# Performance work log

Measured on AMD Instinct MI355X. Metric: run time of the kernel, lower is better.

Reference implementation:

```python
import jax, jax.numpy as jnp
import numpy as np

# PyTorch LSTM gate order: i, f, g, o. Dropout layers are identity in eval mode.

def _lstm_step(w_ih, w_hh, b):
    def step(carry, xt):
        h, c = carry
        g = xt @ w_ih.T + h @ w_hh.T + b
        i, f, gg, o = jnp.split(g, 4, axis=-1)
        c = jax.nn.sigmoid(f) * c + jax.nn.sigmoid(i) * jnp.tanh(gg)
        h = jax.nn.sigmoid(o) * jnp.tanh(c)
        return (h, c), h
    return step


def bilstm(x, wf_ih, wf_hh, bf_ih, bf_hh, wb_ih, wb_hh, bb_ih, bb_hh):
    # x: [B, T, D] -> out: [B, T, 2H]
    B = x.shape[0]
    H = wf_hh.shape[1]
    xt = jnp.swapaxes(x, 0, 1)  # [T, B, D]
    init = (jnp.zeros((B, H), x.dtype), jnp.zeros((B, H), x.dtype))
    _, hf = jax.lax.scan(_lstm_step(wf_ih, wf_hh, bf_ih + bf_hh), init, xt)
    _, hb = jax.lax.scan(_lstm_step(wb_ih, wb_hh, bb_ih + bb_hh), init, xt[::-1])
    hb = hb[::-1]
    return jnp.swapaxes(jnp.concatenate([hf, hb], axis=-1), 0, 1)


def setup_inputs() -> dict:
    key = jax.random.key(0)
    ks = iter(jax.random.split(key, 64))
    d = {"x": jax.random.normal(next(ks), (1024, 1024, 8), jnp.float32)}
    layer_dims = [(16, 20), (40, 20), (40, 10), (20, 10)]
    for li, (din, H) in enumerate(layer_dims, start=1):
        for dr in ("f", "b"):
            d[f"w{li}{dr}_ih"] = 0.1 * jax.random.normal(next(ks), (4 * H, din), jnp.float32)
            d[f"w{li}{dr}_hh"] = 0.1 * jax.random.normal(next(ks), (4 * H, H), jnp.float32)
            d[f"b{li}{dr}_ih"] = 0.1 * jax.random.normal(next(ks), (4 * H,), jnp.float32)
            d[f"b{li}{dr}_hh"] = 0.1 * jax.random.normal(next(ks), (4 * H,), jnp.float32)
    d["fc_w"] = 0.1 * jax.random.normal(next(ks), (1, 20), jnp.float32)
    d["fc_b"] = 0.1 * jax.random.normal(next(ks), (1,), jnp.float32)
    return d


def reference(x,
              w1f_ih, w1f_hh, b1f_ih, b1f_hh, w1b_ih, w1b_hh, b1b_ih, b1b_hh,
              w2f_ih, w2f_hh, b2f_ih, b2f_hh, w2b_ih, w2b_hh, b2b_ih, b2b_hh,
              w3f_ih, w3f_hh, b3f_ih, b3f_hh, w3b_ih, w3b_hh, b3b_ih, b3b_hh,
              w4f_ih, w4f_hh, b4f_ih, b4f_hh, w4b_ih, w4b_hh, b4b_ih, b4b_hh,
              fc_w, fc_b):
    # lag-1 concat: [B,T,8] -> [B,T,16]
    x_lag = jnp.concatenate([jnp.zeros_like(x[:, :1, :]), x[:, :-1, :]], axis=1)
    h = jnp.concatenate([x, x_lag], axis=2)
    h = bilstm(h, w1f_ih, w1f_hh, b1f_ih, b1f_hh, w1b_ih, w1b_hh, b1b_ih, b1b_hh)
    h = bilstm(h, w2f_ih, w2f_hh, b2f_ih, b2f_hh, w2b_ih, w2b_hh, b2b_ih, b2b_hh)
    h = bilstm(h, w3f_ih, w3f_hh, b3f_ih, b3f_hh, w3b_ih, w3b_hh, b3b_ih, b3b_hh)
    h = bilstm(h, w4f_ih, w4f_hh, b4f_ih, b4f_hh, w4b_ih, w4b_hh, b4b_ih, b4b_hh)
    h = h[:, -1, :]  # [B, 20]
    return jax.nn.sigmoid(h @ fc_w.T + fc_b)
```

## Files before the change

### kernel.cpp

```cpp
#include <hip/hip_runtime.h>
#include <hip/hip_fp16.h>
#include <stdint.h>

#define B_TOTAL 1024
#define T_TOTAL 1024
#define LOG2E 1.44269504088896f

typedef _Float16 f16x2 __attribute__((ext_vector_type(2)));

__device__ __forceinline__ float dot2w(uint32_t xw, uint32_t ww, float acc) {
#if __has_builtin(__builtin_amdgcn_fdot2)
    return __builtin_amdgcn_fdot2(__builtin_bit_cast(f16x2, xw),
                                  __builtin_bit_cast(f16x2, ww), acc, false);
#else
    f16x2 xv = __builtin_bit_cast(f16x2, xw);
    f16x2 wv = __builtin_bit_cast(f16x2, ww);
    return acc + (float)xv.x * (float)wv.x + (float)xv.y * (float)wv.y;
#endif
}

__device__ __forceinline__ uint32_t packf2(float a, float b) {
    f16x2 t;
    t.x = (_Float16)a;
    t.y = (_Float16)b;
    return __builtin_bit_cast(uint32_t, t);
}

__device__ __forceinline__ float sigm_(float z) {
    float e = __builtin_amdgcn_exp2f(-LOG2E * z);
    return __builtin_amdgcn_rcpf(1.0f + e);
}
__device__ __forceinline__ float tanh_(float z) {
    float e = __builtin_amdgcn_exp2f((2.0f * LOG2E) * z);
    float r = __builtin_amdgcn_rcpf(1.0f + e);
    return __builtin_fmaf(-2.0f, r, 1.0f);
}

__device__ __forceinline__ void wavebar() {
#if __has_builtin(__builtin_amdgcn_wave_barrier)
    __builtin_amdgcn_wave_barrier();
#endif
}

template <int DIN, int H, int NDIR, bool L1X>
__global__ void __launch_bounds__(256) proj_kernel(
    const float* __restrict__ x,
    const __half* __restrict__ inbuf,
    const float* __restrict__ w0,
    const float* __restrict__ w1,
    __half* __restrict__ g0,
    __half* __restrict__ g1,
    int t0, int seglen)
{
    constexpr int NDW = DIN / 2;
    constexpr int O4H = 4 * H;
    constexpr int ODW = O4H / 2;
    constexpr int RPB = 16;
    constexpr int TPR = 16;
    constexpr int OPT = (O4H + TPR - 1) / TPR;
    constexpr int TILES = 8;

    __shared__ uint32_t wt[NDW][O4H];
    __shared__ uint32_t xin[RPB * NDW];
    __shared__ uint32_t osm[RPB][ODW];

    const int tid  = threadIdx.x;
    const int dirz = (NDIR == 2) ? (int)blockIdx.y : 0;
    const float* w = dirz ? w1 : w0;
    __half* gout   = dirz ? g1 : g0;
    (void)seglen;

    for (int idx = tid; idx < NDW * O4H; idx += 256) {
        const int d  = idx / O4H;
        const int o  = idx - d * O4H;
        const int jj = o >> 2;
        const int qq = o & 3;
        wt[d][o] = packf2(w[(qq * H + jj) * DIN + 2 * d],
                          w[(qq * H + jj) * DIN + 2 * d + 1]);
    }

    const int rr = tid >> 4;
    const int li = tid & 15;

    for (int tile = 0; tile < TILES; ++tile) {
        const int r0 = ((int)blockIdx.x * TILES + tile) * RPB;
        __syncthreads();

        for (int idx = tid; idx < RPB * NDW; idx += 256) {
            const int r  = r0 + idx / NDW;
            const int d  = idx % NDW;
            const int i  = r >> 10;
            const int bb = r & (B_TOTAL - 1);
            const int t  = dirz ? (T_TOTAL - 1 - t0 - i) : (t0 + i);
            uint32_t v;
            if constexpr (L1X) {
                float2 u = {0.f, 0.f};
                if (d < 4)
                    u = ((const float2*)(x + ((size_t)bb * T_TOTAL + t) * 8))[d];
                else if (t > 0)
                    u = ((const float2*)(x + ((size_t)bb * T_TOTAL + (t - 1)) * 8))[d - 4];
                v = packf2(u.x, u.y);
            } else {
                v = ((const uint32_t*)inbuf)[((size_t)t * B_TOTAL + bb) * NDW + d];
            }
            xin[idx] = v;
        }
        __syncthreads();

        float acc[OPT];
#pragma unroll
        for (int oi = 0; oi < OPT; ++oi) acc[oi] = 0.f;
#pragma unroll
        for (int d = 0; d < NDW; ++d) {
            const uint32_t xv = xin[rr * NDW + d];
#pragma unroll
            for (int oi = 0; oi < OPT; ++oi) {
                const int o = li + oi * TPR;
                if (O4H % TPR == 0 || o < O4H)
                    acc[oi] = dot2w(xv, wt[d][o], acc[oi]);
            }
        }
        {
            __half* oh = (__half*)&osm[rr][0];
#pragma unroll
            for (int oi = 0; oi < OPT; ++oi) {
                const int o = li + oi * TPR;
                if (O4H % TPR == 0 || o < O4H) oh[o] = __float2half(acc[oi]);
            }
        }
        __syncthreads();

        {
            uint32_t* dst = (uint32_t*)gout;
            for (int idx = tid; idx < RPB * ODW; idx += 256) {
                const int r  = idx / ODW;
                const int od = idx - r * ODW;
                dst[(size_t)(r0 + r) * ODW + od] = osm[r][od];
            }
        }
    }
}

template <int H, bool STORE_ALL>
__global__ void __launch_bounds__(64)
__attribute__((amdgpu_waves_per_eu(1, 1))) lstm_scan2(
    const __half* __restrict__ gxf, const __half* __restrict__ gxb,
    const float* __restrict__ whhf, const float* __restrict__ bihf,
    const float* __restrict__ bhhf,
    const float* __restrict__ whhb, const float* __restrict__ bihb,
    const float* __restrict__ bhhb,
    __half* __restrict__ outbuf,
    float* __restrict__ lasth,
    float* __restrict__ sth, float* __restrict__ stc,
    int t0, int seglen)
{
    constexpr int GPW   = 64 / H;
    constexpr int NH    = H / 2;
    constexpr int HS_DW = (H == 20) ? 12 : 8;
    constexpr int PF    = 8;

    const int dir  = blockIdx.y;
    const int lane = threadIdx.x;
    const int g    = lane / H;
    const int j    = lane - g * H;
    const int b    = blockIdx.x * GPW + g;
    const bool valid = (g < GPW) && (b < B_TOTAL);
    const int bs   = valid ? b : (B_TOTAL - 1);

    const __half* gx  = dir ? gxb : gxf;
    const float* w_hh = dir ? whhb : whhf;
    const float* b_i  = dir ? bihb : bihf;
    const float* b_h  = dir ? bhhb : bhhf;

    __shared__ uint32_t hsm[GPW + 1][HS_DW];

    uint32_t whh2[4][NH];
    float bias[4];
#pragma unroll
    for (int q = 0; q < 4; ++q) {
        const int r = q * H + j;
#pragma unroll
        for (int k = 0; k < NH; ++k)
            whh2[q][k] = packf2(w_hh[r * H + 2 * k], w_hh[r * H + 2 * k + 1]);
        bias[q] = b_i[r] + b_h[r];
    }
#pragma unroll
    for (int q = 0; q < 4; ++q) {
#pragma unroll
        for (int k = 0; k < NH; ++k) asm volatile("" : "+v"(whh2[q][k]));
        asm volatile("" : "+v"(bias[q]));
    }

    float c_st, h0;
    if (t0 == 0) {
        c_st = 0.f;
        h0   = 0.f;
    } else {
        h0   = sth[((size_t)dir * B_TOTAL + bs) * H + j];
        c_st = stc[((size_t)dir * B_TOTAL + bs) * H + j];
    }
    ((__half*)&hsm[g][0])[j] = __float2half(h0);
    wavebar();

    uint32_t hd[NH];
    auto readhd = [&]() {
        const uint32_t* hp = &hsm[g][0];
        if constexpr (NH == 10) {
            uint4 v0 = *(const uint4*)hp;
            uint4 v1 = *(const uint4*)(hp + 4);
            uint2 v2 = *(const uint2*)(hp + 8);
            hd[0] = v0.x; hd[1] = v0.y; hd[2] = v0.z; hd[3] = v0.w;
            hd[4] = v1.x; hd[5] = v1.y; hd[6] = v1.z; hd[7] = v1.w;
            hd[8] = v2.x; hd[9] = v2.y;
        } else {
            uint4 v0 = *(const uint4*)hp;
            hd[0] = v0.x; hd[1] = v0.y; hd[2] = v0.z; hd[3] = v0.w;
            hd[4] = hp[4];
        }
    };
    readhd();

    const char*  gb   = (const char*)gx + ((size_t)bs * (4 * H) + (size_t)j * 4) * 2;
    const size_t ISTR = (size_t)B_TOTAL * (4 * H) * 2;

    uint2 pf[PF];
#pragma unroll
    for (int i2 = 0; i2 < PF; ++i2) {
        const int ip = (i2 < seglen) ? i2 : (seglen - 1);
        pf[i2] = *(const uint2*)(gb + (size_t)ip * ISTR);
    }

    __half* op = nullptr;
    ptrdiff_t opstep = 0;
    if constexpr (STORE_ALL) {
        const int tstart = dir ? (T_TOTAL - 1 - t0) : t0;
        op = outbuf + (size_t)tstart * (B_TOTAL * 2 * H) + (size_t)bs * (2 * H) + dir * H + j;
        opstep = (dir ? -1 : 1) * (ptrdiff_t)(B_TOTAL * 2 * H);
    }

    float hlast = h0;

#define STEP(I)                                                               \
    {                                                                         \
        const uint2 gv = pf[I];                                               \
        int ip = sb + (I) + PF;                                               \
        ip = (ip < seglen) ? ip : (seglen - 1);                               \
        pf[I] = *(const uint2*)(gb + (size_t)ip * ISTR);                      \
        const f16x2 p01 = __builtin_bit_cast(f16x2, gv.x);                    \
        const f16x2 p23 = __builtin_bit_cast(f16x2, gv.y);                    \
        float a0 = (float)p01.x + bias[0];                                    \
        float a1 = (float)p01.y + bias[1];                                    \
        float a2 = (float)p23.x + bias[2];                                    \
        float a3 = (float)p23.y + bias[3];                                    \
        _Pragma("unroll")                                                     \
        for (int k = 0; k < NH; ++k) {                                        \
            a0 = dot2w(hd[k], whh2[0][k], a0);                                \
            a1 = dot2w(hd[k], whh2[1][k], a1);                                \
            a2 = dot2w(hd[k], whh2[2][k], a2);                                \
            a3 = dot2w(hd[k], whh2[3][k], a3);                                \
        }                                                                     \
        const float iv = sigm_(a0);                                           \
        const float fv = sigm_(a1);                                           \
        const float gv2 = tanh_(a2);                                          \
        const float ov = sigm_(a3);                                           \
        c_st = __builtin_fmaf(fv, c_st, iv * gv2);                            \
        const float h = ov * tanh_(c_st);                                     \
        ((__half*)&hsm[g][0])[j] = __float2half(h);                           \
        wavebar();                                                            \
        readhd();                                                             \
        hlast = h;                                                            \
        if constexpr (STORE_ALL) {                                            \
            if (valid) *op = __float2half(h);                                 \
            op += opstep;                                                     \
        }                                                                     \
    }

    for (int sb = 0; sb < seglen; sb += PF) {
        STEP(0) STEP(1) STEP(2) STEP(3) STEP(4) STEP(5) STEP(6) STEP(7)
    }
#undef STEP

    if (valid) {
        sth[((size_t)dir * B_TOTAL + b) * H + j] = hlast;
        stc[((size_t)dir * B_TOTAL + b) * H + j] = c_st;
        if constexpr (!STORE_ALL) lasth[b * H + j] = hlast;
    }
}

__global__ void final_kernel(const __half* __restrict__ l3out,
                             const float* __restrict__ hf4,
                             const float* __restrict__ w_ih,
                             const float* __restrict__ b_ih,
                             const float* __restrict__ b_hh,
                             const float* __restrict__ fc_w,
                             const float* __restrict__ fc_b,
                             float* __restrict__ out)
{
    const int b = blockIdx.x * blockDim.x + threadIdx.x;
    if (b >= B_TOTAL) return;

    float in4[20];
    const __half* p = l3out + (size_t)(T_TOTAL - 1) * (B_TOTAL * 20) + (size_t)b * 20;
#pragma unroll
    for (int i = 0; i < 20; ++i) in4[i] = __half2float(p[i]);

    float z = fc_b[0];
#pragma unroll
    for (int k = 0; k < 10; ++k) z += fc_w[k] * hf4[b * 10 + k];

#pragma unroll
    for (int k = 0; k < 10; ++k) {
        float gi = b_ih[k]      + b_hh[k];
        float gg = b_ih[20 + k] + b_hh[20 + k];
        float go = b_ih[30 + k] + b_hh[30 + k];
#pragma unroll
        for (int i = 0; i < 20; ++i) {
            const float xi = in4[i];
            gi += w_ih[k * 20 + i]        * xi;
            gg += w_ih[(20 + k) * 20 + i] * xi;
            go += w_ih[(30 + k) * 20 + i] * xi;
        }
        const float cc = sigm_(gi) * tanh_(gg);
        const float hb = sigm_(go) * tanh_(cc);
        z += fc_w[10 + k] * hb;
    }
    out[b] = sigm_(z);
}

extern "C" void kernel_launch(void* const* d_in, const int* in_sizes, int n_in,
                              void* d_out, int out_size, void* d_ws, size_t ws_size,
                              hipStream_t stream) {
    const float* x = (const float*)d_in[0];
    auto W = [&](int li, int dr, int k) -> const float* {
        return (const float*)d_in[1 + (li - 1) * 8 + dr * 4 + k];
    };
    const float* fc_w = (const float*)d_in[33];
    const float* fc_b = (const float*)d_in[34];
    float* out = (float*)d_out;

    const size_t HA_B = (size_t)T_TOTAL * B_TOTAL * 40 * 2;
    const size_t HB_B = (size_t)T_TOTAL * B_TOTAL * 20 * 2;
    const size_t ST_B = 2ull * B_TOTAL * 20 * 4;
    const size_t F4_B = (size_t)B_TOTAL * 10 * 4;

    char* p = (char*)d_ws;
    __half* hA = (__half*)p;  p += HA_B;
    __half* hB = (__half*)p;  p += HB_B;
    float* sth = (float*)p;   p += ST_B;
    float* stc = (float*)p;   p += ST_B;
    float* hf4 = (float*)p;   p += F4_B;
    __half* gx = (__half*)p;

    const size_t base = HA_B + HB_B + 2 * ST_B + F4_B;
    int SEG = 64;
    if      (ws_size >= base + 1024ull * 327680) SEG = 1024;
    else if (ws_size >= base +  512ull * 327680) SEG = 512;
    else if (ws_size >= base +  256ull * 327680) SEG = 256;
    else if (ws_size >= base +  128ull * 327680) SEG = 128;
    const int nseg = T_TOTAL / SEG;

    auto g1of = [&](int H) { return gx + (size_t)SEG * 1024 * 4 * H; };

    for (int s = 0; s < nseg; ++s) {
        proj_kernel<16, 20, 2, true><<<dim3(SEG * 8, 2), 256, 0, stream>>>(
            x, nullptr, W(1,0,0), W(1,1,0), gx, g1of(20), s * SEG, SEG);
        lstm_scan2<20, true><<<dim3(342, 2), 64, 0, stream>>>(
            gx, g1of(20), W(1,0,1), W(1,0,2), W(1,0,3),
                          W(1,1,1), W(1,1,2), W(1,1,3),
            hA, nullptr, sth, stc, s * SEG, SEG);
    }
    for (int s = 0; s < nseg; ++s) {
        proj_kernel<40, 20, 2, false><<<dim3(SEG * 8, 2), 256, 0, stream>>>(
            nullptr, hA, W(2,0,0), W(2,1,0), gx, g1of(20), s * SEG, SEG);
        lstm_scan2<20, true><<<dim3(342, 2), 64, 0, stream>>>(
            gx, g1of(20), W(2,0,1), W(2,0,2), W(2,0,3),
                          W(2,1,1), W(2,1,2), W(2,1,3),
            hA, nullptr, sth, stc, s * SEG, SEG);
    }
    for (int s = 0; s < nseg; ++s) {
        proj_kernel<40, 10, 2, false><<<dim3(SEG * 8, 2), 256, 0, stream>>>(
            nullptr, hA, W(3,0,0), W(3,1,0), gx, g1of(10), s * SEG, SEG);
        lstm_scan2<10, true><<<dim3(171, 2), 64, 0, stream>>>(
            gx, g1of(10), W(3,0,1), W(3,0,2), W(3,0,3),
                          W(3,1,1), W(3,1,2), W(3,1,3),
            hB, nullptr, sth, stc, s * SEG, SEG);
    }
    for (int s = 0; s < nseg; ++s) {
        proj_kernel<20, 10, 1, false><<<dim3(SEG * 8, 1), 256, 0, stream>>>(
            nullptr, hB, W(4,0,0), W(4,0,0), gx, gx, s * SEG, SEG);
        lstm_scan2<10, false><<<dim3(171, 1), 64, 0, stream>>>(
            gx, gx, W(4,0,1), W(4,0,2), W(4,0,3),
                    W(4,0,1), W(4,0,2), W(4,0,3),
            nullptr, hf4, sth, stc, s * SEG, SEG);
    }

    final_kernel<<<dim3(4), 256, 0, stream>>>(
        hB, hf4, W(4,1,0), W(4,1,2), W(4,1,3), fc_w, fc_b, out);
}
```

Before: 1.801 ms.

## Interleave two independent batch groups per wave in LSTM scan, register-cache projection weights

Result: slower. 2.463 ms (+36.8%).

```diff
diff --git a/kernel.cpp b/kernel.cpp
--- a/kernel.cpp
+++ b/kernel.cpp
@@ -52,16 +52,17 @@
     __half* __restrict__ g1,
     int t0, int seglen)
 {
-    constexpr int NDW = DIN / 2;
-    constexpr int O4H = 4 * H;
-    constexpr int ODW = O4H / 2;
-    constexpr int RPB = 16;
-    constexpr int TPR = 16;
-    constexpr int OPT = (O4H + TPR - 1) / TPR;
+    constexpr int NDW  = DIN / 2;
+    constexpr int XPAD = (NDW + 3) & ~3;
+    constexpr int O4H  = 4 * H;
+    constexpr int ODW  = O4H / 2;
+    constexpr int RPB  = 16;
+    constexpr int TPR  = 16;
+    constexpr int OPT  = (O4H + TPR - 1) / TPR;
     constexpr int TILES = 8;
 
     __shared__ uint32_t wt[NDW][O4H];
-    __shared__ uint32_t xin[RPB * NDW];
+    __shared__ uint32_t xin[RPB * XPAD];
     __shared__ uint32_t osm[RPB][ODW];
 
     const int tid  = threadIdx.x;
@@ -78,17 +79,28 @@
         wt[d][o] = packf2(w[(qq * H + jj) * DIN + 2 * d],
                           w[(qq * H + jj) * DIN + 2 * d + 1]);
     }
+    __syncthreads();
 
     const int rr = tid >> 4;
     const int li = tid & 15;
+
+    uint32_t wreg[NDW][OPT];
+#pragma unroll
+    for (int d = 0; d < NDW; ++d)
+#pragma unroll
+        for (int oi = 0; oi < OPT; ++oi) {
+            const int o = li + oi * TPR;
+            wreg[d][oi] = (O4H % TPR == 0 || o < O4H) ? wt[d][o] : 0u;
+        }
 
     for (int tile = 0; tile < TILES; ++tile) {
         const int r0 = ((int)blockIdx.x * TILES + tile) * RPB;
         __syncthreads();
 
         for (int idx = tid; idx < RPB * NDW; idx += 256) {
-            const int r  = r0 + idx / NDW;
-            const int d  = idx % NDW;
+            const int rl = idx / NDW;
+            const int d  = idx - rl * NDW;
+            const int r  = r0 + rl;
             const int i  = r >> 10;
             const int bb = r & (B_TOTAL - 1);
             const int t  = dirz ? (T_TOTAL - 1 - t0 - i) : (t0 + i);
@@ -103,21 +115,32 @@
             } else {
                 v = ((const uint32_t*)inbuf)[((size_t)t * B_TOTAL + bb) * NDW + d];
             }
-            xin[idx] = v;
+            xin[rl * XPAD + d] = v;
         }
         __syncthreads();
 
         float acc[OPT];
 #pragma unroll
         for (int oi = 0; oi < OPT; ++oi) acc[oi] = 0.f;
-#pragma unroll
-        for (int d = 0; d < NDW; ++d) {
-            const uint32_t xv = xin[rr * NDW + d];
+        const uint32_t* xr = &xin[rr * XPAD];
+#pragma unroll
+        for (int d = 0; d + 4 <= NDW; d += 4) {
+            const uint4 xv = *(const uint4*)(xr + d);
 #pragma unroll
             for (int oi = 0; oi < OPT; ++oi) {
-                const int o = li + oi * TPR;
-                if (O4H % TPR == 0 || o < O4H)
-                    acc[oi] = dot2w(xv, wt[d][o], acc[oi]);
+                acc[oi] = dot2w(xv.x, wreg[d][oi], acc[oi]);
+                acc[oi] = dot2w(xv.y, wreg[d + 1][oi], acc[oi]);
+                acc[oi] = dot2w(xv.z, wreg[d + 2][oi], acc[oi]);
+                acc[oi] = dot2w(xv.w, wreg[d + 3][oi], acc[oi]);
+            }
+        }
+        if constexpr ((NDW & 3) >= 2) {
+            constexpr int d0 = NDW & ~3;
+            const uint2 xv = *(const uint2*)(xr + d0);
+#pragma unroll
+            for (int oi = 0; oi < OPT; ++oi) {
+                acc[oi] = dot2w(xv.x, wreg[d0][oi], acc[oi]);
+                acc[oi] = dot2w(xv.y, wreg[d0 + 1][oi], acc[oi]);
             }
         }
         {
@@ -155,24 +178,28 @@
     int t0, int seglen)
 {
     constexpr int GPW   = 64 / H;
+    constexpr int NB    = 2 * GPW;
     constexpr int NH    = H / 2;
     constexpr int HS_DW = (H == 20) ? 12 : 8;
-    constexpr int PF    = 8;
+    constexpr int PFD   = 4;
 
     const int dir  = blockIdx.y;
     const int lane = threadIdx.x;
     const int g    = lane / H;
     const int j    = lane - g * H;
-    const int b    = blockIdx.x * GPW + g;
-    const bool valid = (g < GPW) && (b < B_TOTAL);
-    const int bs   = valid ? b : (B_TOTAL - 1);
+    const int bA   = blockIdx.x * NB + g;
+    const int bB   = blockIdx.x * NB + GPW + g;
+    const bool vA  = (g < GPW) && (bA < B_TOTAL);
+    const bool vB  = (g < GPW) && (bB < B_TOTAL);
+    const int bsA  = vA ? bA : (B_TOTAL - 1);
+    const int bsB  = vB ? bB : (B_TOTAL - 1);
 
     const __half* gx  = dir ? gxb : gxf;
     const float* w_hh = dir ? whhb : whhf;
     const float* b_i  = dir ? bihb : bihf;
     const float* b_h  = dir ? bhhb : bhhf;
 
-    __shared__ uint32_t hsm[GPW + 1][HS_DW];
+    __shared__ uint32_t hsm[2][GPW + 1][HS_DW];
 
     uint32_t whh2[4][NH];
     float bias[4];
@@ -191,61 +218,69 @@
         asm volatile("" : "+v"(bias[q]));
     }
 
-    float c_st, h0;
+    float cA, h0A, cB, h0B;
     if (t0 == 0) {
-        c_st = 0.f;
-        h0   = 0.f;
+        cA = h0A = cB = h0B = 0.f;
     } else {
-        h0   = sth[((size_t)dir * B_TOTAL + bs) * H + j];
-        c_st = stc[((size_t)dir * B_TOTAL + bs) * H + j];
-    }
-    ((__half*)&hsm[g][0])[j] = __float2half(h0);
+        h0A = sth[((size_t)dir * B_TOTAL + bsA) * H + j];
+        cA  = stc[((size_t)dir * B_TOTAL + bsA) * H + j];
+        h0B = sth[((size_t)dir * B_TOTAL + bsB) * H + j];
+        cB  = stc[((size_t)dir * B_TOTAL + bsB) * H + j];
+    }
+    ((__half*)&hsm[0][g][0])[j] = __float2half(h0A);
+    ((__half*)&hsm[1][g][0])[j] = __float2half(h0B);
     wavebar();
 
-    uint32_t hd[NH];
-    auto readhd = [&]() {
-        const uint32_t* hp = &hsm[g][0];
-        if constexpr (NH == 10) {
-            uint4 v0 = *(const uint4*)hp;
-            uint4 v1 = *(const uint4*)(hp + 4);
-            uint2 v2 = *(const uint2*)(hp + 8);
-            hd[0] = v0.x; hd[1] = v0.y; hd[2] = v0.z; hd[3] = v0.w;
-            hd[4] = v1.x; hd[5] = v1.y; hd[6] = v1.z; hd[7] = v1.w;
-            hd[8] = v2.x; hd[9] = v2.y;
-        } else {
-            uint4 v0 = *(const uint4*)hp;
-            hd[0] = v0.x; hd[1] = v0.y; hd[2] = v0.z; hd[3] = v0.w;
-            hd[4] = hp[4];
-        }
-    };
-    readhd();
-
-    const char*  gb   = (const char*)gx + ((size_t)bs * (4 * H) + (size_t)j * 4) * 2;
+    uint32_t hdA[NH], hdB[NH];
+
+#define READHD(hd, S)                                                         \
+    {                                                                         \
+        const uint32_t* hp = &hsm[S][g][0];                                   \
+        if constexpr (NH == 10) {                                             \
+            uint4 v0 = *(const uint4*)hp;                                     \
+            uint4 v1 = *(const uint4*)(hp + 4);                               \
+            uint2 v2 = *(const uint2*)(hp + 8);                               \
+            hd[0] = v0.x; hd[1] = v0.y; hd[2] = v0.z; hd[3] = v0.w;           \
+            hd[4] = v1.x; hd[5] = v1.y; hd[6] = v1.z; hd[7] = v1.w;           \
+            hd[8] = v2.x; hd[9] = v2.y;                                       \
+        } else {                                                              \
+            uint4 v0 = *(const uint4*)hp;                                     \
+            hd[0] = v0.x; hd[1] = v0.y; hd[2] = v0.z; hd[3] = v0.w;           \
+            hd[4] = hp[4];                                                    \
+        }                                                                     \
+    }
+
+    READHD(hdA, 0)
+
     const size_t ISTR = (size_t)B_TOTAL * (4 * H) * 2;
-
-    uint2 pf[PF];
-#pragma unroll
-    for (int i2 = 0; i2 < PF; ++i2) {
+    const char* gbA = (const char*)gx + ((size_t)bsA * (4 * H) + (size_t)j * 4) * 2;
+    const char* gbB = (const char*)gx + ((size_t)bsB * (4 * H) + (size_t)j * 4) * 2;
+
+    uint2 pfA[PFD], pfB[PFD];
+#pragma unroll
+    for (int i2 = 0; i2 < PFD; ++i2) {
         const int ip = (i2 < seglen) ? i2 : (seglen - 1);
-        pf[i2] = *(const uint2*)(gb + (size_t)ip * ISTR);
-    }
-
-    __half* op = nullptr;
+        pfA[i2] = *(const uint2*)(gbA + (size_t)ip * ISTR);
+        pfB[i2] = *(const uint2*)(gbB + (size_t)ip * ISTR);
+    }
+
+    __half *opA = nullptr, *opB = nullptr;
     ptrdiff_t opstep = 0;
     if constexpr (STORE_ALL) {
         const int tstart = dir ? (T_TOTAL - 1 - t0) : t0;
-        op = outbuf + (size_t)tstart * (B_TOTAL * 2 * H) + (size_t)bs * (2 * H) + dir * H + j;
+        opA = outbuf + (size_t)tstart * (B_TOTAL * 2 * H) + (size_t)bsA * (2 * H) + dir * H + j;
+        opB = outbuf + (size_t)tstart * (B_TOTAL * 2 * H) + (size_t)bsB * (2 * H) + dir * H + j;
         opstep = (dir ? -1 : 1) * (ptrdiff_t)(B_TOTAL * 2 * H);
     }
 
-    float hlast = h0;
-
-#define STEP(I)                                                               \
+    float hlA = h0A, hlB = h0B;
+
+#define PHASE(hd, pfr, gbp, cst, opp, hl, VV, S, I)                           \
     {                                                                         \
-        const uint2 gv = pf[I];                                               \
-        int ip = sb + (I) + PF;                                               \
+        const uint2 gv = pfr[I];                                              \
+        int ip = sb + (I) + PFD;                                              \
         ip = (ip < seglen) ? ip : (seglen - 1);                               \
-        pf[I] = *(const uint2*)(gb + (size_t)ip * ISTR);                      \
+        pfr[I] = *(const uint2*)(gbp + (size_t)ip * ISTR);                    \
         const f16x2 p01 = __builtin_bit_cast(f16x2, gv.x);                    \
         const f16x2 p23 = __builtin_bit_cast(f16x2, gv.y);                    \
         float a0 = (float)p01.x + bias[0];                                    \
@@ -259,31 +294,44 @@
             a2 = dot2w(hd[k], whh2[2][k], a2);                                \
             a3 = dot2w(hd[k], whh2[3][k], a3);                                \
         }                                                                     \
-        const float iv = sigm_(a0);                                           \
-        const float fv = sigm_(a1);                                           \
-        const float gv2 = tanh_(a2);                                          \
-        const float ov = sigm_(a3);                                           \
-        c_st = __builtin_fmaf(fv, c_st, iv * gv2);                            \
-        const float h = ov * tanh_(c_st);                                     \
-        ((__half*)&hsm[g][0])[j] = __float2half(h);                           \
-        wavebar();                                                            \
-        readhd();                                                             \
-        hlast = h;                                                            \
+        const float iv  = sigm_(a0);                                          \
+        const float fv  = sigm_(a1);                                          \
+        const float gg2 = tanh_(a2);                                          \
+        const float ov  = sigm_(a3);                                          \
+        cst = __builtin_fmaf(fv, cst, iv * gg2);                              \
+        const float hh = ov * tanh_(cst);                                     \
+        ((__half*)&hsm[S][g][0])[j] = __float2half(hh);                       \
+        hl = hh;                                                              \
         if constexpr (STORE_ALL) {                                            \
-            if (valid) *op = __float2half(h);                                 \
-            op += opstep;                                                     \
+            if (VV) *opp = __float2half(hh);                                  \
+            opp += opstep;                                                    \
         }                                                                     \
     }
 
-    for (int sb = 0; sb < seglen; sb += PF) {
-        STEP(0) STEP(1) STEP(2) STEP(3) STEP(4) STEP(5) STEP(6) STEP(7)
-    }
-#undef STEP
-
-    if (valid) {
-        sth[((size_t)dir * B_TOTAL + b) * H + j] = hlast;
-        stc[((size_t)dir * B_TOTAL + b) * H + j] = c_st;
-        if constexpr (!STORE_ALL) lasth[b * H + j] = hlast;
+#define ITER(I)                                                               \
+    wavebar();                                                                \
+    READHD(hdB, 1)                                                            \
+    PHASE(hdA, pfA, gbA, cA, opA, hlA, vA, 0, I)                              \
+    wavebar();                                                                \
+    READHD(hdA, 0)                                                            \
+    PHASE(hdB, pfB, gbB, cB, opB, hlB, vB, 1, I)
+
+    for (int sb = 0; sb < seglen; sb += PFD) {
+        ITER(0) ITER(1) ITER(2) ITER(3)
+    }
+#undef ITER
+#undef PHASE
+#undef READHD
+
+    if (vA) {
+        sth[((size_t)dir * B_TOTAL + bA) * H + j] = hlA;
+        stc[((size_t)dir * B_TOTAL + bA) * H + j] = cA;
+        if constexpr (!STORE_ALL) lasth[bA * H + j] = hlA;
+    }
+    if (vB) {
+        sth[((size_t)dir * B_TOTAL + bB) * H + j] = hlB;
+        stc[((size_t)dir * B_TOTAL + bB) * H + j] = cB;
+        if constexpr (!STORE_ALL) lasth[bB * H + j] = hlB;
     }
 }
 
@@ -364,7 +412,7 @@
     for (int s = 0; s < nseg; ++s) {
         proj_kernel<16, 20, 2, true><<<dim3(SEG * 8, 2), 256, 0, stream>>>(
             x, nullptr, W(1,0,0), W(1,1,0), gx, g1of(20), s * SEG, SEG);
-        lstm_scan2<20, true><<<dim3(342, 2), 64, 0, stream>>>(
+        lstm_scan2<20, true><<<dim3(171, 2), 64, 0, stream>>>(
             gx, g1of(20), W(1,0,1), W(1,0,2), W(1,0,3),
                           W(1,1,1), W(1,1,2), W(1,1,3),
             hA, nullptr, sth, stc, s * SEG, SEG);
@@ -372,7 +420,7 @@
     for (int s = 0; s < nseg; ++s) {
         proj_kernel<40, 20, 2, false><<<dim3(SEG * 8, 2), 256, 0, stream>>>(
             nullptr, hA, W(2,0,0), W(2,1,0), gx, g1of(20), s * SEG, SEG);
-        lstm_scan2<20, true><<<dim3(342, 2), 64, 0, stream>>>(
+        lstm_scan2<20, true><<<dim3(171, 2), 64, 0, stream>>>(
             gx, g1of(20), W(2,0,1), W(2,0,2), W(2,0,3),
                           W(2,1,1), W(2,1,2), W(2,1,3),
             hA, nullptr, sth, stc, s * SEG, SEG);
@@ -380,7 +428,7 @@
     for (int s = 0; s < nseg; ++s) {
         proj_kernel<40, 10, 2, false><<<dim3(SEG * 8, 2), 256, 0, stream>>>(
             nullptr, hA, W(3,0,0), W(3,1,0), gx, g1of(10), s * SEG, SEG);
-        lstm_scan2<10, true><<<dim3(171, 2), 64, 0, stream>>>(
+        lstm_scan2<10, true><<<dim3(86, 2), 64, 0, stream>>>(
             gx, g1of(10), W(3,0,1), W(3,0,2), W(3,0,3),
                           W(3,1,1), W(3,1,2), W(3,1,3),
             hB, nullptr, sth, stc, s * SEG, SEG);
@@ -388,7 +436,7 @@
     for (int s = 0; s < nseg; ++s) {
         proj_kernel<20, 10, 1, false><<<dim3(SEG * 8, 1), 256, 0, stream>>>(
             nullptr, hB, W(4,0,0), W(4,0,0), gx, gx, s * SEG, SEG);
-        lstm_scan2<10, false><<<dim3(171, 1), 64, 0, stream>>>(
+        lstm_scan2<10, false><<<dim3(86, 1), 64, 0, stream>>>(
             gx, gx, W(4,0,1), W(4,0,2), W(4,0,3),
                     W(4,0,1), W(4,0,2), W(4,0,3),
             nullptr, hf4, sth, stc, s * SEG, SEG);
```

## Stage gate inputs through LDS and batch h stores in LSTM scan

Applied to the files above, without the earlier changes.

Result: slower. 2.114 ms (+17.4%).

```diff
diff --git a/kernel.cpp b/kernel.cpp
--- a/kernel.cpp
+++ b/kernel.cpp
@@ -52,17 +52,18 @@
     __half* __restrict__ g1,
     int t0, int seglen)
 {
-    constexpr int NDW = DIN / 2;
-    constexpr int O4H = 4 * H;
-    constexpr int ODW = O4H / 2;
-    constexpr int RPB = 16;
-    constexpr int TPR = 16;
-    constexpr int OPT = (O4H + TPR - 1) / TPR;
+    constexpr int NDW  = DIN / 2;
+    constexpr int XPAD = (NDW + 3) & ~3;
+    constexpr int O4H  = 4 * H;
+    constexpr int ODW  = O4H / 2;
+    constexpr int RPB  = 16;
+    constexpr int TPR  = 16;
+    constexpr int OPT  = (O4H + TPR - 1) / TPR;
     constexpr int TILES = 8;
 
-    __shared__ uint32_t wt[NDW][O4H];
-    __shared__ uint32_t xin[RPB * NDW];
-    __shared__ uint32_t osm[RPB][ODW];
+    __shared__ __align__(16) uint32_t wt[NDW][O4H];
+    __shared__ __align__(16) uint32_t xin[RPB * XPAD];
+    __shared__ __align__(16) uint32_t osm[RPB][ODW];
 
     const int tid  = threadIdx.x;
     const int dirz = (NDIR == 2) ? (int)blockIdx.y : 0;
@@ -78,17 +79,28 @@
         wt[d][o] = packf2(w[(qq * H + jj) * DIN + 2 * d],
                           w[(qq * H + jj) * DIN + 2 * d + 1]);
     }
+    __syncthreads();
 
     const int rr = tid >> 4;
     const int li = tid & 15;
+
+    uint32_t wreg[NDW][OPT];
+#pragma unroll
+    for (int d = 0; d < NDW; ++d)
+#pragma unroll
+        for (int oi = 0; oi < OPT; ++oi) {
+            const int o = li + oi * TPR;
+            wreg[d][oi] = (O4H % TPR == 0 || o < O4H) ? wt[d][o] : 0u;
+        }
 
     for (int tile = 0; tile < TILES; ++tile) {
         const int r0 = ((int)blockIdx.x * TILES + tile) * RPB;
         __syncthreads();
 
         for (int idx = tid; idx < RPB * NDW; idx += 256) {
-            const int r  = r0 + idx / NDW;
-            const int d  = idx % NDW;
+            const int rl = idx / NDW;
+            const int d  = idx - rl * NDW;
+            const int r  = r0 + rl;
             const int i  = r >> 10;
             const int bb = r & (B_TOTAL - 1);
             const int t  = dirz ? (T_TOTAL - 1 - t0 - i) : (t0 + i);
@@ -103,21 +115,32 @@
             } else {
                 v = ((const uint32_t*)inbuf)[((size_t)t * B_TOTAL + bb) * NDW + d];
             }
-            xin[idx] = v;
+            xin[rl * XPAD + d] = v;
         }
         __syncthreads();
 
         float acc[OPT];
 #pragma unroll
         for (int oi = 0; oi < OPT; ++oi) acc[oi] = 0.f;
-#pragma unroll
-        for (int d = 0; d < NDW; ++d) {
-            const uint32_t xv = xin[rr * NDW + d];
+        const uint32_t* xr = &xin[rr * XPAD];
+#pragma unroll
+        for (int d = 0; d + 4 <= NDW; d += 4) {
+            const uint4 xv = *(const uint4*)(xr + d);
 #pragma unroll
             for (int oi = 0; oi < OPT; ++oi) {
-                const int o = li + oi * TPR;
-                if (O4H % TPR == 0 || o < O4H)
-                    acc[oi] = dot2w(xv, wt[d][o], acc[oi]);
+                acc[oi] = dot2w(xv.x, wreg[d][oi], acc[oi]);
+                acc[oi] = dot2w(xv.y, wreg[d + 1][oi], acc[oi]);
+                acc[oi] = dot2w(xv.z, wreg[d + 2][oi], acc[oi]);
+                acc[oi] = dot2w(xv.w, wreg[d + 3][oi], acc[oi]);
+            }
+        }
+        if constexpr ((NDW & 3) >= 2) {
+            constexpr int d0 = NDW & ~3;
+            const uint2 xv = *(const uint2*)(xr + d0);
+#pragma unroll
+            for (int oi = 0; oi < OPT; ++oi) {
+                acc[oi] = dot2w(xv.x, wreg[d0][oi], acc[oi]);
+                acc[oi] = dot2w(xv.y, wreg[d0 + 1][oi], acc[oi]);
             }
         }
         {
@@ -143,7 +166,7 @@
 
 template <int H, bool STORE_ALL>
 __global__ void __launch_bounds__(64)
-__attribute__((amdgpu_waves_per_eu(1, 1))) lstm_scan2(
+__attribute__((amdgpu_waves_per_eu(1, 1))) lstm_scan3(
     const __half* __restrict__ gxf, const __half* __restrict__ gxb,
     const float* __restrict__ whhf, const float* __restrict__ bihf,
     const float* __restrict__ bhhf,
@@ -156,13 +179,15 @@
 {
     constexpr int GPW   = 64 / H;
     constexpr int NH    = H / 2;
-    constexpr int HS_DW = (H == 20) ? 12 : 8;
-    constexpr int PF    = 8;
+    constexpr int PADH  = (H == 20) ? 24 : 12;
+    constexpr int B8H   = 8 * H;
+    constexpr int SLICE = GPW * B8H;
 
     const int dir  = blockIdx.y;
     const int lane = threadIdx.x;
     const int g    = lane / H;
     const int j    = lane - g * H;
+    const int gs   = (g < GPW) ? g : (GPW - 1);
     const int b    = blockIdx.x * GPW + g;
     const bool valid = (g < GPW) && (b < B_TOTAL);
     const int bs   = valid ? b : (B_TOTAL - 1);
@@ -172,7 +197,8 @@
     const float* b_i  = dir ? bihb : bihf;
     const float* b_h  = dir ? bhhb : bhhf;
 
-    __shared__ uint32_t hsm[GPW + 1][HS_DW];
+    __shared__ __align__(16) uint32_t gxs[2][16 * 120];
+    __shared__ __align__(16) __half hout[16][80];
 
     uint32_t whh2[4][NH];
     float bias[4];
@@ -190,6 +216,52 @@
         for (int k = 0; k < NH; ++k) asm volatile("" : "+v"(whh2[q][k]));
         asm volatile("" : "+v"(bias[q]));
     }
+
+    const size_t ISTR = (size_t)B_TOTAL * B8H;
+    const uint32_t boff = (uint32_t)blockIdx.x * SLICE;
+    const uint32_t SL = (uint32_t)(((size_t)boff + SLICE <= ISTR) ? SLICE
+                                                                  : (ISTR - boff));
+    const int sub = lane >> 5, l32 = lane & 31;
+    const uint32_t loff = (uint32_t)l32 * 16;
+    const uint32_t offc = (loff < SL) ? loff : 0u;
+    const char* gxc = (const char*)gx;
+
+    uint4 greg[8];
+    auto issue_loads = [&](int cbase) {
+#pragma unroll
+        for (int r = 0; r < 8; ++r) {
+            const int i = 2 * r + sub;
+            greg[r] = *(const uint4*)(gxc + (size_t)(cbase + i) * ISTR + boff + offc);
+        }
+    };
+    auto write_stage = [&](int bb) {
+        if (loff < SL) {
+#pragma unroll
+            for (int r = 0; r < 8; ++r) {
+                const int i = 2 * r + sub;
+                *(uint4*)((char*)&gxs[bb][0] + (size_t)i * 480 + loff) = greg[r];
+            }
+        }
+    };
+
+    uint32_t hd[NH];
+    auto read_hd = [&](int row) {
+        const char* hp = (const char*)&hout[0][0] + row * 160 + gs * (PADH * 2);
+        if constexpr (H == 20) {
+            uint4 v0 = *(const uint4*)hp;
+            uint4 v1 = *(const uint4*)(hp + 16);
+            uint2 v2 = *(const uint2*)(hp + 32);
+            hd[0] = v0.x; hd[1] = v0.y; hd[2] = v0.z; hd[3] = v0.w;
+            hd[4] = v1.x; hd[5] = v1.y; hd[6] = v1.z; hd[7] = v1.w;
+            hd[8] = v2.x; hd[9] = v2.y;
+        } else {
+            uint2 v0 = *(const uint2*)hp;
+            uint2 v1 = *(const uint2*)(hp + 8);
+            hd[0] = v0.x; hd[1] = v0.y; hd[2] = v1.x; hd[3] = v1.y;
+            hd[4] = *(const uint32_t*)(hp + 16);
+        }
+    };
+    const int hoff = (g < GPW) ? (gs * PADH + j) : (72 + (lane & 7));
 
     float c_st, h0;
     if (t0 == 0) {
@@ -199,91 +271,106 @@
         h0   = sth[((size_t)dir * B_TOTAL + bs) * H + j];
         c_st = stc[((size_t)dir * B_TOTAL + bs) * H + j];
     }
-    ((__half*)&hsm[g][0])[j] = __float2half(h0);
+    *(__half*)((char*)&hout[0][0] + 15 * 160 + hoff * 2) = __float2half(h0);
     wavebar();
-
-    uint32_t hd[NH];
-    auto readhd = [&]() {
-        const uint32_t* hp = &hsm[g][0];
-        if constexpr (NH == 10) {
-            uint4 v0 = *(const uint4*)hp;
-            uint4 v1 = *(const uint4*)(hp + 4);
-            uint2 v2 = *(const uint2*)(hp + 8);
-            hd[0] = v0.x; hd[1] = v0.y; hd[2] = v0.z; hd[3] = v0.w;
-            hd[4] = v1.x; hd[5] = v1.y; hd[6] = v1.z; hd[7] = v1.w;
-            hd[8] = v2.x; hd[9] = v2.y;
-        } else {
-            uint4 v0 = *(const uint4*)hp;
-            hd[0] = v0.x; hd[1] = v0.y; hd[2] = v0.z; hd[3] = v0.w;
-            hd[4] = hp[4];
-        }
-    };
-    readhd();
-
-    const char*  gb   = (const char*)gx + ((size_t)bs * (4 * H) + (size_t)j * 4) * 2;
-    const size_t ISTR = (size_t)B_TOTAL * (4 * H) * 2;
-
-    uint2 pf[PF];
-#pragma unroll
-    for (int i2 = 0; i2 < PF; ++i2) {
-        const int ip = (i2 < seglen) ? i2 : (seglen - 1);
-        pf[i2] = *(const uint2*)(gb + (size_t)ip * ISTR);
-    }
-
-    __half* op = nullptr;
-    ptrdiff_t opstep = 0;
-    if constexpr (STORE_ALL) {
-        const int tstart = dir ? (T_TOTAL - 1 - t0) : t0;
-        op = outbuf + (size_t)tstart * (B_TOTAL * 2 * H) + (size_t)bs * (2 * H) + dir * H + j;
-        opstep = (dir ? -1 : 1) * (ptrdiff_t)(B_TOTAL * 2 * H);
-    }
-
-    float hlast = h0;
-
-#define STEP(I)                                                               \
-    {                                                                         \
-        const uint2 gv = pf[I];                                               \
-        int ip = sb + (I) + PF;                                               \
-        ip = (ip < seglen) ? ip : (seglen - 1);                               \
-        pf[I] = *(const uint2*)(gb + (size_t)ip * ISTR);                      \
-        const f16x2 p01 = __builtin_bit_cast(f16x2, gv.x);                    \
-        const f16x2 p23 = __builtin_bit_cast(f16x2, gv.y);                    \
-        float a0 = (float)p01.x + bias[0];                                    \
-        float a1 = (float)p01.y + bias[1];                                    \
-        float a2 = (float)p23.x + bias[2];                                    \
-        float a3 = (float)p23.y + bias[3];                                    \
-        _Pragma("unroll")                                                     \
-        for (int k = 0; k < NH; ++k) {                                        \
-            a0 = dot2w(hd[k], whh2[0][k], a0);                                \
-            a1 = dot2w(hd[k], whh2[1][k], a1);                                \
-            a2 = dot2w(hd[k], whh2[2][k], a2);                                \
-            a3 = dot2w(hd[k], whh2[3][k], a3);                                \
-        }                                                                     \
-        const float iv = sigm_(a0);                                           \
-        const float fv = sigm_(a1);                                           \
-        const float gv2 = tanh_(a2);                                          \
-        const float ov = sigm_(a3);                                           \
-        c_st = __builtin_fmaf(fv, c_st, iv * gv2);                            \
-        const float h = ov * tanh_(c_st);                                     \
-        ((__half*)&hsm[g][0])[j] = __float2half(h);                           \
-        wavebar();                                                            \
-        readhd();                                                             \
-        hlast = h;                                                            \
-        if constexpr (STORE_ALL) {                                            \
-            if (valid) *op = __float2half(h);                                 \
-            op += opstep;                                                     \
-        }                                                                     \
-    }
-
-    for (int sb = 0; sb < seglen; sb += PF) {
-        STEP(0) STEP(1) STEP(2) STEP(3) STEP(4) STEP(5) STEP(6) STEP(7)
-    }
-#undef STEP
+    read_hd(15);
+
+    issue_loads(0);
+    write_stage(0);
+    issue_loads(16);
+    wavebar();
+
+    const int gxrd = gs * (2 * H) + j * 2;
+    uint2 gxcur = *(const uint2*)((const char*)&gxs[0][0] + gxrd * 4);
+    uint2 gxn;
+
+    float hl = h0;
+
+    auto step = [&](int i, int cur) {
+        const int nrow = (i < 15) ? (i + 1) : 0;
+        const int nbuf = (i < 15) ? cur : (cur ^ 1);
+        gxn = *(const uint2*)((const char*)&gxs[nbuf][0] + nrow * 480 + gxrd * 4);
+
+        const f16x2 p01 = __builtin_bit_cast(f16x2, gxcur.x);
+        const f16x2 p23 = __builtin_bit_cast(f16x2, gxcur.y);
+        float a0 = (float)p01.x + bias[0];
+        float a1 = (float)p01.y + bias[1];
+        float a2 = (float)p23.x + bias[2];
+        float a3 = (float)p23.y + bias[3];
+        float e0 = 0.f, e1 = 0.f, e2 = 0.f, e3 = 0.f;
+#pragma unroll
+        for (int k = 0; k < NH / 2; ++k) {
+            a0 = dot2w(hd[k], whh2[0][k], a0);
+            a1 = dot2w(hd[k], whh2[1][k], a1);
+            a2 = dot2w(hd[k], whh2[2][k], a2);
+            a3 = dot2w(hd[k], whh2[3][k], a3);
+        }
+#pragma unroll
+        for (int k = NH / 2; k < NH; ++k) {
+            e0 = dot2w(hd[k], whh2[0][k], e0);
+            e1 = dot2w(hd[k], whh2[1][k], e1);
+            e2 = dot2w(hd[k], whh2[2][k], e2);
+            e3 = dot2w(hd[k], whh2[3][k], e3);
+        }
+        a0 += e0; a1 += e1; a2 += e2; a3 += e3;
+
+        const float iv  = sigm_(a0);
+        const float fv  = sigm_(a1);
+        const float gg2 = tanh_(a2);
+        const float ov  = sigm_(a3);
+        c_st = __builtin_fmaf(fv, c_st, iv * gg2);
+        const float h = ov * tanh_(c_st);
+
+        *(__half*)((char*)&hout[0][0] + i * 160 + hoff * 2) = __float2half(h);
+        wavebar();
+        read_hd(i);
+        gxcur = gxn;
+        hl = h;
+    };
+
+    auto flush = [&](int cb) {
+        if constexpr (STORE_ALL) {
+#pragma unroll
+            for (int r = 0; r < 8; ++r) {
+                const int fd = r * 64 + lane;
+                if (fd < 480) {
+                    const int t  = fd / 30;
+                    const int w  = fd - t * 30;
+                    const int gg = w / NH;
+                    const int kk = w - gg * NH;
+                    const uint32_t hv = *(const uint32_t*)((const char*)&hout[0][0] +
+                                          t * 160 + (gg * PADH + 2 * kk) * 2);
+                    const int bb2 = blockIdx.x * GPW + gg;
+                    if (bb2 < B_TOTAL) {
+                        const int tg = dir ? (T_TOTAL - 1 - (t0 + cb + t))
+                                           : (t0 + cb + t);
+                        *(uint32_t*)((char*)outbuf +
+                            ((size_t)tg * (B_TOTAL * 2 * H) +
+                             (size_t)bb2 * (2 * H) + dir * H) * 2 + kk * 4) = hv;
+                    }
+                }
+            }
+        }
+    };
+
+    const int nch = seglen / 16;
+    int cur = 0;
+    for (int c = 0; c < nch; ++c) {
+        const int cb = c * 16;
+#pragma unroll
+        for (int i = 0; i < 8; ++i) step(i, cur);
+        if (c + 1 < nch) write_stage(cur ^ 1);
+#pragma unroll
+        for (int i = 8; i < 16; ++i) step(i, cur);
+        flush(cb);
+        if (c + 2 < nch) issue_loads(cb + 32);
+        cur ^= 1;
+    }
 
     if (valid) {
-        sth[((size_t)dir * B_TOTAL + b) * H + j] = hlast;
+        sth[((size_t)dir * B_TOTAL + b) * H + j] = hl;
         stc[((size_t)dir * B_TOTAL + b) * H + j] = c_st;
-        if constexpr (!STORE_ALL) lasth[b * H + j] = hlast;
+        if constexpr (!STORE_ALL) lasth[b * H + j] = hl;
     }
 }
 
@@ -364,7 +451,7 @@
     for (int s = 0; s < nseg; ++s) {
         proj_kernel<16, 20, 2, true><<<dim3(SEG * 8, 2), 256, 0, stream>>>(
             x, nullptr, W(1,0,0), W(1,1,0), gx, g1of(20), s * SEG, SEG);
-        lstm_scan2<20, true><<<dim3(342, 2), 64, 0, stream>>>(
+        lstm_scan3<20, true><<<dim3(342, 2), 64, 0, stream>>>(
             gx, g1of(20), W(1,0,1), W(1,0,2), W(1,0,3),
                           W(1,1,1), W(1,1,2), W(1,1,3),
             hA, nullptr, sth, stc, s * SEG, SEG);
@@ -372,7 +459,7 @@
     for (int s = 0; s < nseg; ++s) {
         proj_kernel<40, 20, 2, false><<<dim3(SEG * 8, 2), 256, 0, stream>>>(
             nullptr, hA, W(2,0,0), W(2,1,0), gx, g1of(20), s * SEG, SEG);
-        lstm_scan2<20, true><<<dim3(342, 2), 64, 0, stream>>>(
+        lstm_scan3<20, true><<<dim3(342, 2), 64, 0, stream>>>(
             gx, g1of(20), W(2,0,1), W(2,0,2), W(2,0,3),
                           W(2,1,1), W(2,1,2), W(2,1,3),
             hA, nullptr, sth, stc, s * SEG, SEG);
@@ -380,7 +467,7 @@
     for (int s = 0; s < nseg; ++s) {
         proj_kernel<40, 10, 2, false><<<dim3(SEG * 8, 2), 256, 0, stream>>>(
             nullptr, hA, W(3,0,0), W(3,1,0), gx, g1of(10), s * SEG, SEG);
-        lstm_scan2<10, true><<<dim3(171, 2), 64, 0, stream>>>(
+        lstm_scan3<10, true><<<dim3(171, 2), 64, 0, stream>>>(
             gx, g1of(10), W(3,0,1), W(3,0,2), W(3,0,3),
                           W(3,1,1), W(3,1,2), W(3,1,3),
             hB, nullptr, sth, stc, s * SEG, SEG);
@@ -388,7 +475,7 @@
     for (int s = 0; s < nseg; ++s) {
         proj_kernel<20, 10, 1, false><<<dim3(SEG * 8, 1), 256, 0, stream>>>(
             nullptr, hB, W(4,0,0), W(4,0,0), gx, gx, s * SEG, SEG);
-        lstm_scan2<10, false><<<dim3(171, 1), 64, 0, stream>>>(
+        lstm_scan3<10, false><<<dim3(171, 1), 64, 0, stream>>>(
             gx, gx, W(4,0,1), W(4,0,2), W(4,0,3),
                     W(4,0,1), W(4,0,2), W(4,0,3),
             nullptr, hf4, sth, stc, s * SEG, SEG);
```

## Exchange LSTM hidden state via DPP/bpermute and cache projection weights in registers

Applied to the files above, without the earlier changes.

Result: slower. 1.929 ms (+7.1%).

```diff
diff --git a/kernel.cpp b/kernel.cpp
--- a/kernel.cpp
+++ b/kernel.cpp
@@ -34,12 +34,6 @@
     float e = __builtin_amdgcn_exp2f((2.0f * LOG2E) * z);
     float r = __builtin_amdgcn_rcpf(1.0f + e);
     return __builtin_fmaf(-2.0f, r, 1.0f);
-}
-
-__device__ __forceinline__ void wavebar() {
-#if __has_builtin(__builtin_amdgcn_wave_barrier)
-    __builtin_amdgcn_wave_barrier();
-#endif
 }
 
 template <int DIN, int H, int NDIR, bool L1X>
@@ -52,17 +46,18 @@
     __half* __restrict__ g1,
     int t0, int seglen)
 {
-    constexpr int NDW = DIN / 2;
-    constexpr int O4H = 4 * H;
-    constexpr int ODW = O4H / 2;
-    constexpr int RPB = 16;
-    constexpr int TPR = 16;
-    constexpr int OPT = (O4H + TPR - 1) / TPR;
+    constexpr int NDW  = DIN / 2;
+    constexpr int XPAD = (NDW + 3) & ~3;
+    constexpr int O4H  = 4 * H;
+    constexpr int ODW  = O4H / 2;
+    constexpr int RPB  = 16;
+    constexpr int TPR  = 16;
+    constexpr int OPT  = (O4H + TPR - 1) / TPR;
     constexpr int TILES = 8;
 
-    __shared__ uint32_t wt[NDW][O4H];
-    __shared__ uint32_t xin[RPB * NDW];
-    __shared__ uint32_t osm[RPB][ODW];
+    __shared__ __align__(16) uint32_t wt[NDW][O4H];
+    __shared__ __align__(16) uint32_t xin[RPB * XPAD];
+    __shared__ __align__(16) uint32_t osm[RPB][ODW];
 
     const int tid  = threadIdx.x;
     const int dirz = (NDIR == 2) ? (int)blockIdx.y : 0;
@@ -78,17 +73,28 @@
         wt[d][o] = packf2(w[(qq * H + jj) * DIN + 2 * d],
                           w[(qq * H + jj) * DIN + 2 * d + 1]);
     }
+    __syncthreads();
 
     const int rr = tid >> 4;
     const int li = tid & 15;
+
+    uint32_t wreg[NDW][OPT];
+#pragma unroll
+    for (int d = 0; d < NDW; ++d)
+#pragma unroll
+        for (int oi = 0; oi < OPT; ++oi) {
+            const int o = li + oi * TPR;
+            wreg[d][oi] = (O4H % TPR == 0 || o < O4H) ? wt[d][o] : 0u;
+        }
 
     for (int tile = 0; tile < TILES; ++tile) {
         const int r0 = ((int)blockIdx.x * TILES + tile) * RPB;
         __syncthreads();
 
         for (int idx = tid; idx < RPB * NDW; idx += 256) {
-            const int r  = r0 + idx / NDW;
-            const int d  = idx % NDW;
+            const int rl = idx / NDW;
+            const int d  = idx - rl * NDW;
+            const int r  = r0 + rl;
             const int i  = r >> 10;
             const int bb = r & (B_TOTAL - 1);
             const int t  = dirz ? (T_TOTAL - 1 - t0 - i) : (t0 + i);
@@ -103,21 +109,32 @@
             } else {
                 v = ((const uint32_t*)inbuf)[((size_t)t * B_TOTAL + bb) * NDW + d];
             }
-            xin[idx] = v;
+            xin[rl * XPAD + d] = v;
         }
         __syncthreads();
 
         float acc[OPT];
 #pragma unroll
         for (int oi = 0; oi < OPT; ++oi) acc[oi] = 0.f;
-#pragma unroll
-        for (int d = 0; d < NDW; ++d) {
-            const uint32_t xv = xin[rr * NDW + d];
+        const uint32_t* xr = &xin[rr * XPAD];
+#pragma unroll
+        for (int d = 0; d + 4 <= NDW; d += 4) {
+            const uint4 xv = *(const uint4*)(xr + d);
 #pragma unroll
             for (int oi = 0; oi < OPT; ++oi) {
-                const int o = li + oi * TPR;
-                if (O4H % TPR == 0 || o < O4H)
-                    acc[oi] = dot2w(xv, wt[d][o], acc[oi]);
+                acc[oi] = dot2w(xv.x, wreg[d][oi], acc[oi]);
+                acc[oi] = dot2w(xv.y, wreg[d + 1][oi], acc[oi]);
+                acc[oi] = dot2w(xv.z, wreg[d + 2][oi], acc[oi]);
+                acc[oi] = dot2w(xv.w, wreg[d + 3][oi], acc[oi]);
+            }
+        }
+        if constexpr ((NDW & 3) >= 2) {
+            constexpr int d0 = NDW & ~3;
+            const uint2 xv = *(const uint2*)(xr + d0);
+#pragma unroll
+            for (int oi = 0; oi < OPT; ++oi) {
+                acc[oi] = dot2w(xv.x, wreg[d0][oi], acc[oi]);
+                acc[oi] = dot2w(xv.y, wreg[d0 + 1][oi], acc[oi]);
             }
         }
         {
@@ -143,7 +160,7 @@
 
 template <int H, bool STORE_ALL>
 __global__ void __launch_bounds__(64)
-__attribute__((amdgpu_waves_per_eu(1, 1))) lstm_scan2(
+__attribute__((amdgpu_waves_per_eu(1, 1))) lstm_scan4(
     const __half* __restrict__ gxf, const __half* __restrict__ gxb,
     const float* __restrict__ whhf, const float* __restrict__ bihf,
     const float* __restrict__ bhhf,
@@ -154,15 +171,15 @@
     float* __restrict__ sth, float* __restrict__ stc,
     int t0, int seglen)
 {
-    constexpr int GPW   = 64 / H;
-    constexpr int NH    = H / 2;
-    constexpr int HS_DW = (H == 20) ? 12 : 8;
-    constexpr int PF    = 8;
+    constexpr int GPW = 64 / H;
+    constexpr int NH  = H / 2;
+    constexpr int PF  = 4;
 
     const int dir  = blockIdx.y;
     const int lane = threadIdx.x;
     const int g    = lane / H;
     const int j    = lane - g * H;
+    const int gs   = (g < GPW) ? g : (GPW - 1);
     const int b    = blockIdx.x * GPW + g;
     const bool valid = (g < GPW) && (b < B_TOTAL);
     const int bs   = valid ? b : (B_TOTAL - 1);
@@ -172,8 +189,6 @@
     const float* b_i  = dir ? bihb : bihf;
     const float* b_h  = dir ? bhhb : bhhf;
 
-    __shared__ uint32_t hsm[GPW + 1][HS_DW];
-
     uint32_t whh2[4][NH];
     float bias[4];
 #pragma unroll
@@ -190,6 +205,21 @@
         for (int k = 0; k < NH; ++k) asm volatile("" : "+v"(whh2[q][k]));
         asm volatile("" : "+v"(bias[q]));
     }
+
+    const int  base4 = (gs * H) * 4;
+    const bool evn   = ((lane & 1) == 0);
+    uint32_t hd[NH];
+    auto exchange = [&](float h) {
+        const uint32_t hf = (uint32_t)__builtin_bit_cast(uint16_t, (_Float16)h);
+        const uint32_t nb = (uint32_t)__builtin_amdgcn_mov_dpp(
+            (int)hf, 0xB1 , 0xF, 0xF, true);
+        const uint32_t lo = evn ? hf : nb;
+        const uint32_t hi = evn ? nb : hf;
+        const uint32_t pairw = lo | (hi << 16);
+#pragma unroll
+        for (int k = 0; k < NH; ++k)
+            hd[k] = (uint32_t)__builtin_amdgcn_ds_bpermute(base4 + 8 * k, (int)pairw);
+    };
 
     float c_st, h0;
     if (t0 == 0) {
@@ -199,29 +229,10 @@
         h0   = sth[((size_t)dir * B_TOTAL + bs) * H + j];
         c_st = stc[((size_t)dir * B_TOTAL + bs) * H + j];
     }
-    ((__half*)&hsm[g][0])[j] = __float2half(h0);
-    wavebar();
-
-    uint32_t hd[NH];
-    auto readhd = [&]() {
-        const uint32_t* hp = &hsm[g][0];
-        if constexpr (NH == 10) {
-            uint4 v0 = *(const uint4*)hp;
-            uint4 v1 = *(const uint4*)(hp + 4);
-            uint2 v2 = *(const uint2*)(hp + 8);
-            hd[0] = v0.x; hd[1] = v0.y; hd[2] = v0.z; hd[3] = v0.w;
-            hd[4] = v1.x; hd[5] = v1.y; hd[6] = v1.z; hd[7] = v1.w;
-            hd[8] = v2.x; hd[9] = v2.y;
-        } else {
-            uint4 v0 = *(const uint4*)hp;
-            hd[0] = v0.x; hd[1] = v0.y; hd[2] = v0.z; hd[3] = v0.w;
-            hd[4] = hp[4];
-        }
-    };
-    readhd();
-
+    exchange(h0);
+
+    const size_t ISTR = (size_t)B_TOTAL * (4 * H) * 2;
     const char*  gb   = (const char*)gx + ((size_t)bs * (4 * H) + (size_t)j * 4) * 2;
-    const size_t ISTR = (size_t)B_TOTAL * (4 * H) * 2;
 
     uint2 pf[PF];
 #pragma unroll
@@ -238,7 +249,7 @@
         opstep = (dir ? -1 : 1) * (ptrdiff_t)(B_TOTAL * 2 * H);
     }
 
-    float hlast = h0;
+    float hl = h0;
 
 #define STEP(I)                                                               \
     {                                                                         \
@@ -259,31 +270,29 @@
             a2 = dot2w(hd[k], whh2[2][k], a2);                                \
             a3 = dot2w(hd[k], whh2[3][k], a3);                                \
         }                                                                     \
-        const float iv = sigm_(a0);                                           \
-        const float fv = sigm_(a1);                                           \
-        const float gv2 = tanh_(a2);                                          \
-        const float ov = sigm_(a3);                                           \
-        c_st = __builtin_fmaf(fv, c_st, iv * gv2);                            \
+        const float iv  = sigm_(a0);                                          \
+        const float fv  = sigm_(a1);                                          \
+        const float gg2 = tanh_(a2);                                          \
+        const float ov  = sigm_(a3);                                          \
+        c_st = __builtin_fmaf(fv, c_st, iv * gg2);                            \
         const float h = ov * tanh_(c_st);                                     \
-        ((__half*)&hsm[g][0])[j] = __float2half(h);                           \
-        wavebar();                                                            \
-        readhd();                                                             \
-        hlast = h;                                                            \
         if constexpr (STORE_ALL) {                                            \
             if (valid) *op = __float2half(h);                                 \
             op += opstep;                                                     \
         }                                                                     \
+        exchange(h);                                                          \
+        hl = h;                                                               \
     }
 
     for (int sb = 0; sb < seglen; sb += PF) {
-        STEP(0) STEP(1) STEP(2) STEP(3) STEP(4) STEP(5) STEP(6) STEP(7)
+        STEP(0) STEP(1) STEP(2) STEP(3)
     }
 #undef STEP
 
     if (valid) {
-        sth[((size_t)dir * B_TOTAL + b) * H + j] = hlast;
+        sth[((size_t)dir * B_TOTAL + b) * H + j] = hl;
         stc[((size_t)dir * B_TOTAL + b) * H + j] = c_st;
-        if constexpr (!STORE_ALL) lasth[b * H + j] = hlast;
+        if constexpr (!STORE_ALL) lasth[b * H + j] = hl;
     }
 }
 
@@ -364,7 +373,7 @@
     for (int s = 0; s < nseg; ++s) {
         proj_kernel<16, 20, 2, true><<<dim3(SEG * 8, 2), 256, 0, stream>>>(
             x, nullptr, W(1,0,0), W(1,1,0), gx, g1of(20), s * SEG, SEG);
-        lstm_scan2<20, true><<<dim3(342, 2), 64, 0, stream>>>(
+        lstm_scan4<20, true><<<dim3(342, 2), 64, 0, stream>>>(
             gx, g1of(20), W(1,0,1), W(1,0,2), W(1,0,3),
                           W(1,1,1), W(1,1,2), W(1,1,3),
             hA, nullptr, sth, stc, s * SEG, SEG);
@@ -372,7 +381,7 @@
     for (int s = 0; s < nseg; ++s) {
         proj_kernel<40, 20, 2, false><<<dim3(SEG * 8, 2), 256, 0, stream>>>(
             nullptr, hA, W(2,0,0), W(2,1,0), gx, g1of(20), s * SEG, SEG);
-        lstm_scan2<20, true><<<dim3(342, 2), 64, 0, stream>>>(
+        lstm_scan4<20, true><<<dim3(342, 2), 64, 0, stream>>>(
             gx, g1of(20), W(2,0,1), W(2,0,2), W(2,0,3),
                           W(2,1,1), W(2,1,2), W(2,1,3),
             hA, nullptr, sth, stc, s * SEG, SEG);
@@ -380,7 +389,7 @@
     for (int s = 0; s < nseg; ++s) {
         proj_kernel<40, 10, 2, false><<<dim3(SEG * 8, 2), 256, 0, stream>>>(
             nullptr, hA, W(3,0,0), W(3,1,0), gx, g1of(10), s * SEG, SEG);
-        lstm_scan2<10, true><<<dim3(171, 2), 64, 0, stream>>>(
+        lstm_scan4<10, true><<<dim3(171, 2), 64, 0, stream>>>(
             gx, g1of(10), W(3,0,1), W(3,0,2), W(3,0,3),
                           W(3,1,1), W(3,1,2), W(3,1,3),
             hB, nullptr, sth, stc, s * SEG, SEG);
@@ -388,7 +397,7 @@
     for (int s = 0; s < nseg; ++s) {
         proj_kernel<20, 10, 1, false><<<dim3(SEG * 8, 1), 256, 0, stream>>>(
             nullptr, hB, W(4,0,0), W(4,0,0), gx, gx, s * SEG, SEG);
-        lstm_scan2<10, false><<<dim3(171, 1), 64, 0, stream>>>(
+        lstm_scan4<10, false><<<dim3(171, 1), 64, 0, stream>>>(
             gx, gx, W(4,0,1), W(4,0,2), W(4,0,3),
                     W(4,0,1), W(4,0,2), W(4,0,3),
             nullptr, hf4, sth, stc, s * SEG, SEG);
```
